# Kernel tuning notes

Hardware: AMD Instinct MI355X
Metric: run time of the kernel (lower is better)

The kernel has to match this reference:

```python
import jax, jax.numpy as jnp
import numpy as np

B, C, W, H = 4, 128, 64, 64
CK = 32  # f/g projection channels


def setup_inputs() -> dict:
    key = jax.random.key(0)
    ks = jax.random.split(key, 8)
    s_in = 1.0 / np.sqrt(C)
    return {
        "x": jax.random.normal(ks[0], (B, C, W, H), dtype=jnp.float32),
        "Wf": jax.random.normal(ks[1], (CK, C), dtype=jnp.float32) * s_in,
        "bf": jnp.zeros((CK,), dtype=jnp.float32),
        "Wg": jax.random.normal(ks[2], (CK, C), dtype=jnp.float32) * s_in,
        "bg": jnp.zeros((CK,), dtype=jnp.float32),
        "Wh": jax.random.normal(ks[3], (C, C), dtype=jnp.float32) * s_in,
        "bh": jnp.zeros((C,), dtype=jnp.float32),
        "gamma": jax.random.normal(ks[4], (1,), dtype=jnp.float32) * 0.1,
    }


def reference(x, Wf, bf, Wg, bg, Wh, bh, gamma):
    b, c, w, h = x.shape
    n = w * h
    xf = x.reshape(b, c, n)                                  # [B,C,N]
    # 1x1 convs == per-pixel linear projections
    f = jnp.einsum('oc,bcn->bon', Wf, xf) + bf[None, :, None]  # [B,32,N]
    g = jnp.einsum('oc,bcn->bon', Wg, xf) + bg[None, :, None]  # [B,32,N]
    v = jnp.einsum('oc,bcn->bon', Wh, xf) + bh[None, :, None]  # [B,C,N]
    # attention = softmax(f^T g) over last dim (g positions), as in the torch code
    att = jax.nn.softmax(jnp.einsum('bkn,bkm->bnm', f, g), axis=-1)  # [B,N,N]
    # self_attention = h @ attention  (contract over f-position axis)
    sa = jnp.einsum('bcn,bnm->bcm', v, att).reshape(b, c, w, h)
    return gamma[0] * sa + x
```

## Files before the change

kernel.cpp:

```cpp
#include <hip/hip_runtime.h>
#include <hip/hip_bf16.h>

#define BB 4
#define CC 128
#define NN 4096
#define CK 32
#define L2E 1.442695040888963f

typedef __attribute__((ext_vector_type(8))) short short8v;
typedef __attribute__((ext_vector_type(4))) float float4v;

__device__ inline ushort f2bf(float f) {
    union { __hip_bfloat16 h; ushort u; } cv;
    cv.h = __float2bfloat16(f);
    return cv.u;
}
__device__ inline float bf2f(ushort u) {
    union { uint u; float f; } cv;
    cv.u = ((uint)u) << 16;
    return cv.f;
}
__device__ inline uint pk2(float lo, float hi) {
    return ((uint)f2bf(lo)) | ((uint)f2bf(hi) << 16);
}
__device__ __forceinline__ void gll16(const void* g, void* l) {
    __builtin_amdgcn_global_load_lds(
        (const __attribute__((address_space(1))) void*)g,
        (__attribute__((address_space(3))) void*)l, 16, 0, 0);
}

__global__ __launch_bounds__(1024) void proj_kernel(
    const float* __restrict__ x,
    const float* __restrict__ Wf, const float* __restrict__ bf,
    const float* __restrict__ Wg, const float* __restrict__ bg,
    const float* __restrict__ Wh, const float* __restrict__ bh,
    const float* __restrict__ gamma,
    ushort* __restrict__ ft, ushort* __restrict__ gt, ushort* __restrict__ vh)
{
    __shared__ float xs[CC][64];
    const int t  = threadIdx.x;
    const int n0 = blockIdx.x * 64;
    const int b  = blockIdx.y;
    const float* xb = x + (size_t)b * CC * NN + n0;

    {
        const int j  = t & 63;
        const int cb = t >> 6;
        #pragma unroll
        for (int i = 0; i < 8; ++i)
            xs[cb + 16 * i][j] = xb[(size_t)(cb + 16 * i) * NN + j];
    }
    __syncthreads();

    const int jq = t & 15;
    const int og = (t >> 4) & 15;
    const int i3 = t >> 8;

    const float* wrow[3];
    float biasv[3];
    int   mode[3], oc[3];
    #pragma unroll
    for (int ii = 0; ii < 3; ++ii) {
        const int i = i3 * 3 + ii;
        if (i < 2)      { oc[ii] = og + 16 * i;       wrow[ii] = Wf + oc[ii] * CC; biasv[ii] = bf[oc[ii]]; mode[ii] = 0; }
        else if (i < 4) { oc[ii] = og + 16 * (i - 2); wrow[ii] = Wg + oc[ii] * CC; biasv[ii] = bg[oc[ii]]; mode[ii] = 1; }
        else            { oc[ii] = og + 16 * (i - 4); wrow[ii] = Wh + oc[ii] * CC; biasv[ii] = bh[oc[ii]]; mode[ii] = 2; }
    }

    float acc[3][4];
    #pragma unroll
    for (int ii = 0; ii < 3; ++ii)
        #pragma unroll
        for (int jj = 0; jj < 4; ++jj) acc[ii][jj] = 0.f;

    #pragma unroll 4
    for (int c4 = 0; c4 < 32; ++c4) {
        float4 wv[3];
        #pragma unroll
        for (int ii = 0; ii < 3; ++ii)
            wv[ii] = *reinterpret_cast<const float4*>(&wrow[ii][c4 * 4]);
        #pragma unroll
        for (int q = 0; q < 4; ++q) {
            const float4 xv = *reinterpret_cast<const float4*>(&xs[c4 * 4 + q][jq * 4]);
            #pragma unroll
            for (int ii = 0; ii < 3; ++ii) {
                const float wq = (q == 0) ? wv[ii].x : (q == 1) ? wv[ii].y
                               : (q == 2) ? wv[ii].z : wv[ii].w;
                acc[ii][0] += wq * xv.x;
                acc[ii][1] += wq * xv.y;
                acc[ii][2] += wq * xv.z;
                acc[ii][3] += wq * xv.w;
            }
        }
    }

    const float sgn = (gamma[0] < 0.f) ? -1.f : 1.f;
    const int n_base = n0 + jq * 4;
    #pragma unroll
    for (int ii = 0; ii < 3; ++ii) {
        if (mode[ii] == 0) {
            #pragma unroll
            for (int jj = 0; jj < 4; ++jj)
                ft[((size_t)b * NN + n_base + jj) * CK + oc[ii]] =
                    f2bf((acc[ii][jj] + biasv[ii]) * L2E);
        } else if (mode[ii] == 1) {
            #pragma unroll
            for (int jj = 0; jj < 4; ++jj)
                gt[((size_t)b * NN + n_base + jj) * CK + oc[ii]] = f2bf(acc[ii][jj] + biasv[ii]);
        } else {
            ushort4 pkv;
            pkv.x = f2bf(sgn * (acc[ii][0] + biasv[ii]));
            pkv.y = f2bf(sgn * (acc[ii][1] + biasv[ii]));
            pkv.z = f2bf(sgn * (acc[ii][2] + biasv[ii]));
            pkv.w = f2bf(sgn * (acc[ii][3] + biasv[ii]));
            *reinterpret_cast<ushort4*>(&vh[((size_t)b * CC + oc[ii]) * NN + n_base]) = pkv;
        }
    }
}

__global__ __launch_bounds__(256) void pass1_kernel(
    const ushort* __restrict__ ft, const ushort* __restrict__ gt,
    float* __restrict__ Dpart)
{
    const int t   = threadIdx.x;
    const int w   = t >> 6;
    const int l   = t & 63;
    const int g16 = l >> 4;
    const int l16 = l & 15;
    const int n0  = blockIdx.x * 64;
    const int b   = blockIdx.y;
    const int mz  = blockIdx.z;

    const ushort* ftb = ft + (size_t)b * NN * CK;
    const ushort* gtb = gt + (size_t)b * NN * CK;

    const short8v afrag = *reinterpret_cast<const short8v*>(
        &ftb[(size_t)(n0 + 16 * w + l16) * CK + 8 * g16]);

    const float4v zf = {0.f, 0.f, 0.f, 0.f};
    float d0 = 0.f, d1 = 0.f, d2 = 0.f, d3 = 0.f;
    const int m0 = mz * 512;

    short8v bfA = *reinterpret_cast<const short8v*>(
        &gtb[(size_t)(m0 + l16) * CK + 8 * g16]);
    #pragma unroll 1
    for (int mt = 0; mt < 32; mt += 2) {
        const short8v bfB = *reinterpret_cast<const short8v*>(
            &gtb[(size_t)(m0 + (mt + 1) * 16 + l16) * CK + 8 * g16]);
        float4v s = __builtin_amdgcn_mfma_f32_16x16x32_bf16(afrag, bfA, zf, 0, 0, 0);
        d0 += __builtin_amdgcn_exp2f(s[0]); d1 += __builtin_amdgcn_exp2f(s[1]);
        d2 += __builtin_amdgcn_exp2f(s[2]); d3 += __builtin_amdgcn_exp2f(s[3]);
        bfA = *reinterpret_cast<const short8v*>(
            &gtb[(size_t)(m0 + (((mt + 2) & 31)) * 16 + l16) * CK + 8 * g16]);
        float4v s2 = __builtin_amdgcn_mfma_f32_16x16x32_bf16(afrag, bfB, zf, 0, 0, 0);
        d0 += __builtin_amdgcn_exp2f(s2[0]); d1 += __builtin_amdgcn_exp2f(s2[1]);
        d2 += __builtin_amdgcn_exp2f(s2[2]); d3 += __builtin_amdgcn_exp2f(s2[3]);
    }
    #pragma unroll
    for (int msk = 1; msk <= 8; msk <<= 1) {
        d0 += __shfl_xor(d0, msk);
        d1 += __shfl_xor(d1, msk);
        d2 += __shfl_xor(d2, msk);
        d3 += __shfl_xor(d3, msk);
    }
    if (l16 < 4) {
        const int n = n0 + 16 * w + 4 * g16 + l16;
        const float v = (l16 == 0) ? d0 : (l16 == 1) ? d1 : (l16 == 2) ? d2 : d3;
        Dpart[((size_t)b * NN + n) * 8 + mz] = v;
    }
}

__global__ __launch_bounds__(256) void reduce_kernel(
    const float* __restrict__ Dpart, float* __restrict__ sc,
    const float* __restrict__ gamma)
{
    const int i = blockIdx.x * 256 + threadIdx.x;
    const float4 a4 = *reinterpret_cast<const float4*>(&Dpart[(size_t)i * 8]);
    const float4 b4 = *reinterpret_cast<const float4*>(&Dpart[(size_t)i * 8 + 4]);
    const float D = (a4.x + a4.y + a4.z + a4.w) + (b4.x + b4.y + b4.z + b4.w);
    sc[i] = fabsf(gamma[0]) / D;
}

__global__ __launch_bounds__(256) void vscale_kernel(
    ushort* __restrict__ vh, const float* __restrict__ sc)
{
    const size_t i8   = (size_t)blockIdx.x * 256 + threadIdx.x;
    const size_t base = i8 * 8;
    const int    n    = (int)(base & (NN - 1));
    const int    b    = (int)(base / ((size_t)CC * NN));

    ushort4 v0 = *reinterpret_cast<const ushort4*>(&vh[base]);
    ushort4 v1 = *reinterpret_cast<const ushort4*>(&vh[base + 4]);
    const float4 s0 = *reinterpret_cast<const float4*>(&sc[(size_t)b * NN + n]);
    const float4 s1 = *reinterpret_cast<const float4*>(&sc[(size_t)b * NN + n + 4]);

    v0.x = f2bf(bf2f(v0.x) * s0.x);
    v0.y = f2bf(bf2f(v0.y) * s0.y);
    v0.z = f2bf(bf2f(v0.z) * s0.z);
    v0.w = f2bf(bf2f(v0.w) * s0.w);
    v1.x = f2bf(bf2f(v1.x) * s1.x);
    v1.y = f2bf(bf2f(v1.y) * s1.y);
    v1.z = f2bf(bf2f(v1.z) * s1.z);
    v1.w = f2bf(bf2f(v1.w) * s1.w);

    *reinterpret_cast<ushort4*>(&vh[base])     = v0;
    *reinterpret_cast<ushort4*>(&vh[base + 4]) = v1;
}

#define WSTR  16384
#define VBUF  8192

__global__ __launch_bounds__(512) void pass2_kernel(
    const ushort* __restrict__ ft, const ushort* __restrict__ gt,
    const ushort* __restrict__ vh,
    const float* __restrict__ x, float* __restrict__ out)
{
    __shared__ __align__(16) char smem[8 * WSTR];

    const int t   = threadIdx.x;
    const int w   = t >> 6;
    const int l   = t & 63;
    const int g16 = l >> 4;
    const int l16 = l & 15;
    const int mq  = w & 1;
    const int nq  = w >> 1;

    const int bid = blockIdx.x;
    const int xcd = bid & 7;
    const int b   = xcd >> 1;
    const int m0  = ((bid >> 3) + 32 * (xcd & 1)) * 64;

    const ushort* ftb = ft + (size_t)b * NN * CK;
    const ushort* gtb = gt + (size_t)b * NN * CK;
    const ushort* vhb = vh + (size_t)b * CC * NN;

    char* wsm = smem + w * WSTR;

    short8v gfrag[2];
    #pragma unroll
    for (int tm = 0; tm < 2; ++tm)
        gfrag[tm] = *reinterpret_cast<const short8v*>(
            &gtb[(size_t)(m0 + 32 * mq + 16 * tm + l16) * CK + 8 * g16]);

    const float4v zf = {0.f, 0.f, 0.f, 0.f};
    float4v acc[8][2];
    #pragma unroll
    for (int tc = 0; tc < 8; ++tc)
        #pragma unroll
        for (int tm = 0; tm < 2; ++tm) acc[tc][tm] = zf;

    const int nbase = nq * 1024;
    const int rr = l >> 2, cp = l & 3;

#define STAGE(n0_, bo_) do {                                                   \
    _Pragma("unroll")                                                          \
    for (int j = 0; j < 8; ++j) {                                              \
        const int row = j * 16 + rr;                                           \
        gll16(vhb + (size_t)row * NN + (n0_)                                   \
                  + (((2 * cp) ^ (row & 6)) << 2),                             \
              wsm + (bo_) + j * 1024);                                         \
    }                                                                          \
} while (0)

    STAGE(nbase, 0);
    asm volatile("s_waitcnt vmcnt(0)" ::: "memory");

    int bo = 0;
    #pragma unroll 1
    for (int st = 0; st < 32; ++st) {
        const int n0 = nbase + st * 32;

        const short8v af0 = *reinterpret_cast<const short8v*>(
            &ftb[(size_t)(n0 + l16) * CK + 8 * g16]);
        const short8v af1 = *reinterpret_cast<const short8v*>(
            &ftb[(size_t)(n0 + 16 + l16) * CK + 8 * g16]);

        if (st < 31) {
            STAGE(n0 + 32, bo ^ VBUF);
            asm volatile("s_waitcnt vmcnt(8)" ::: "memory");
        } else {
            asm volatile("s_waitcnt vmcnt(0)" ::: "memory");
        }

        const char* Vb = wsm + bo;

        union { uint u[4]; short8v s; } pf[2];
        #pragma unroll
        for (int tm = 0; tm < 2; ++tm) {
            float4v s0 = __builtin_amdgcn_mfma_f32_16x16x32_bf16(af0, gfrag[tm], zf, 0, 0, 0);
            float4v s1 = __builtin_amdgcn_mfma_f32_16x16x32_bf16(af1, gfrag[tm], zf, 0, 0, 0);
            pf[tm].u[0] = pk2(__builtin_amdgcn_exp2f(s0[0]), __builtin_amdgcn_exp2f(s0[1]));
            pf[tm].u[1] = pk2(__builtin_amdgcn_exp2f(s0[2]), __builtin_amdgcn_exp2f(s0[3]));
            pf[tm].u[2] = pk2(__builtin_amdgcn_exp2f(s1[0]), __builtin_amdgcn_exp2f(s1[1]));
            pf[tm].u[3] = pk2(__builtin_amdgcn_exp2f(s1[2]), __builtin_amdgcn_exp2f(s1[3]));
        }

        #pragma unroll
        for (int tc = 0; tc < 8; ++tc) {
            const int cl = 16 * tc + l16;
            const uint2 va  = *reinterpret_cast<const uint2*>(
                Vb + cl * 64 + 8 * (g16 ^ (cl & 6)));
            const uint2 vb2 = *reinterpret_cast<const uint2*>(
                Vb + cl * 64 + 8 * ((4 + g16) ^ (cl & 6)));
            union { uint u[4]; short8v s; } av;
            av.u[0] = va.x;  av.u[1] = va.y;
            av.u[2] = vb2.x; av.u[3] = vb2.y;
            acc[tc][0] = __builtin_amdgcn_mfma_f32_16x16x32_bf16(av.s, pf[0].s, acc[tc][0], 0, 0, 0);
            acc[tc][1] = __builtin_amdgcn_mfma_f32_16x16x32_bf16(av.s, pf[1].s, acc[tc][1], 0, 0, 0);
        }
        bo ^= VBUF;
    }
#undef STAGE

    __syncthreads();
    float4v* rl = (float4v*)smem;
    if (nq != 0) {
        const int slot = (nq - 1) * 2 + mq;
        #pragma unroll
        for (int tc = 0; tc < 8; ++tc)
            #pragma unroll
            for (int tm = 0; tm < 2; ++tm)
                rl[(slot * 16 + tc * 2 + tm) * 64 + l] = acc[tc][tm];
    }
    __syncthreads();
    if (nq == 0) {
        const float* xb = x   + (size_t)b * CC * NN;
        float*       ob = out + (size_t)b * CC * NN;
        #pragma unroll
        for (int tc = 0; tc < 8; ++tc) {
            #pragma unroll
            for (int tm = 0; tm < 2; ++tm) {
                const int fi = tc * 2 + tm;
                float4v s = acc[tc][tm]
                          + rl[((mq) * 16 + fi) * 64 + l]
                          + rl[((2 + mq) * 16 + fi) * 64 + l]
                          + rl[((4 + mq) * 16 + fi) * 64 + l];
                const int cb = 16 * tc + 4 * g16;
                const int m  = m0 + 32 * mq + 16 * tm + l16;
                #pragma unroll
                for (int r = 0; r < 4; ++r) {
                    const size_t idx = (size_t)(cb + r) * NN + m;
                    ob[idx] = s[r] + xb[idx];
                }
            }
        }
    }
}

extern "C" void kernel_launch(void* const* d_in, const int* in_sizes, int n_in,
                              void* d_out, int out_size, void* d_ws, size_t ws_size,
                              hipStream_t stream)
{
    const float* x     = (const float*)d_in[0];
    const float* Wf    = (const float*)d_in[1];
    const float* bf    = (const float*)d_in[2];
    const float* Wg    = (const float*)d_in[3];
    const float* bg    = (const float*)d_in[4];
    const float* Wh    = (const float*)d_in[5];
    const float* bh    = (const float*)d_in[6];
    const float* gamma = (const float*)d_in[7];

    ushort* ft = (ushort*)d_ws;
    ushort* gt = ft + (size_t)BB * NN * CK;
    ushort* vh = gt + (size_t)BB * NN * CK;
    float* Dpart = (float*)(vh + (size_t)BB * CC * NN);
    float* sc    = Dpart + (size_t)BB * NN * 8;

    float* out = (float*)d_out;

    proj_kernel<<<dim3(NN / 64, BB), 1024, 0, stream>>>(x, Wf, bf, Wg, bg, Wh, bh, gamma, ft, gt, vh);
    pass1_kernel<<<dim3(NN / 64, BB, 8), 256, 0, stream>>>(ft, gt, Dpart);
    reduce_kernel<<<dim3(BB * NN / 256), 256, 0, stream>>>(Dpart, sc, gamma);
    vscale_kernel<<<dim3(BB * CC * NN / 8 / 256), 256, 0, stream>>>(vh, sc);
    pass2_kernel<<<dim3(256), 512, 0, stream>>>(ft, gt, vh, x, out);
}
```

Baseline: 83.53 us.

## Split pass2 work by channel halves, double grid, and unroll double-buffer loop

The pass2 kernel now gives each wave pair a 32-position m-tile split across two channel halves, where before each wave owned a slice of a 64-position tile. This halves the per-wave accumulators and LDS staging and doubles the grid to 512 blocks, with launch bounds requesting two blocks per CU for better occupancy on a 256-CU device. The main loop is unrolled by two with fixed double-buffer offsets, and the f-fragment loads are prefetched alongside the V staging. The trade-off is that exp/score MFMAs are recomputed by both channel-half waves, doubling that work.

```diff
diff --git a/kernel.cpp b/kernel.cpp
--- a/kernel.cpp
+++ b/kernel.cpp
@@ -207,10 +207,10 @@
     *reinterpret_cast<ushort4*>(&vh[base + 4]) = v1;
 }
 
-#define WSTR  16384
-#define VBUF  8192
-
-__global__ __launch_bounds__(512) void pass2_kernel(
+#define WSTR  8192
+#define VBUF  4096
+
+__global__ __launch_bounds__(512, 2) void pass2_kernel(
     const ushort* __restrict__ ft, const ushort* __restrict__ gt,
     const ushort* __restrict__ vh,
     const float* __restrict__ x, float* __restrict__ out)
@@ -222,13 +222,13 @@
     const int l   = t & 63;
     const int g16 = l >> 4;
     const int l16 = l & 15;
-    const int mq  = w & 1;
+    const int ch  = w & 1;
     const int nq  = w >> 1;
 
     const int bid = blockIdx.x;
     const int xcd = bid & 7;
     const int b   = xcd >> 1;
-    const int m0  = ((bid >> 3) + 32 * (xcd & 1)) * 64;
+    const int m0  = ((bid >> 3) + 64 * (xcd & 1)) * 32;
 
     const ushort* ftb = ft + (size_t)b * NN * CK;
     const ushort* gtb = gt + (size_t)b * NN * CK;
@@ -240,12 +240,12 @@
     #pragma unroll
     for (int tm = 0; tm < 2; ++tm)
         gfrag[tm] = *reinterpret_cast<const short8v*>(
-            &gtb[(size_t)(m0 + 32 * mq + 16 * tm + l16) * CK + 8 * g16]);
+            &gtb[(size_t)(m0 + 16 * tm + l16) * CK + 8 * g16]);
 
     const float4v zf = {0.f, 0.f, 0.f, 0.f};
-    float4v acc[8][2];
-    #pragma unroll
-    for (int tc = 0; tc < 8; ++tc)
+    float4v acc[4][2];
+    #pragma unroll
+    for (int tc = 0; tc < 4; ++tc)
         #pragma unroll
         for (int tm = 0; tm < 2; ++tm) acc[tc][tm] = zf;
 
@@ -254,89 +254,97 @@
 
 #define STAGE(n0_, bo_) do {                                                   \
     _Pragma("unroll")                                                          \
-    for (int j = 0; j < 8; ++j) {                                              \
+    for (int j = 0; j < 4; ++j) {                                              \
         const int row = j * 16 + rr;                                           \
-        gll16(vhb + (size_t)row * NN + (n0_)                                   \
+        gll16(vhb + (size_t)(64 * ch + row) * NN + (n0_)                       \
                   + (((2 * cp) ^ (row & 6)) << 2),                             \
               wsm + (bo_) + j * 1024);                                         \
     }                                                                          \
 } while (0)
 
+#define AFLOAD(A0, A1, n0_) do {                                               \
+    A0 = *reinterpret_cast<const short8v*>(                                    \
+        &ftb[(size_t)((n0_) + l16) * CK + 8 * g16]);                           \
+    A1 = *reinterpret_cast<const short8v*>(                                    \
+        &ftb[(size_t)((n0_) + 16 + l16) * CK + 8 * g16]);                      \
+} while (0)
+
+#define COMPUTE(bo_, A0, A1) do {                                              \
+    const char* Vb = wsm + (bo_);                                              \
+    union { uint u[4]; short8v s; } pf[2];                                     \
+    _Pragma("unroll")                                                          \
+    for (int tm = 0; tm < 2; ++tm) {                                           \
+        float4v s0 = __builtin_amdgcn_mfma_f32_16x16x32_bf16(A0, gfrag[tm], zf, 0, 0, 0); \
+        float4v s1 = __builtin_amdgcn_mfma_f32_16x16x32_bf16(A1, gfrag[tm], zf, 0, 0, 0); \
+        pf[tm].u[0] = pk2(__builtin_amdgcn_exp2f(s0[0]), __builtin_amdgcn_exp2f(s0[1])); \
+        pf[tm].u[1] = pk2(__builtin_amdgcn_exp2f(s0[2]), __builtin_amdgcn_exp2f(s0[3])); \
+        pf[tm].u[2] = pk2(__builtin_amdgcn_exp2f(s1[0]), __builtin_amdgcn_exp2f(s1[1])); \
+        pf[tm].u[3] = pk2(__builtin_amdgcn_exp2f(s1[2]), __builtin_amdgcn_exp2f(s1[3])); \
+    }                                                                          \
+    _Pragma("unroll")                                                          \
+    for (int tc = 0; tc < 4; ++tc) {                                           \
+        const int cl = 16 * tc + l16;                                          \
+        const uint2 va  = *reinterpret_cast<const uint2*>(                     \
+            Vb + cl * 64 + 8 * (g16 ^ (cl & 6)));                              \
+        const uint2 vb2 = *reinterpret_cast<const uint2*>(                     \
+            Vb + cl * 64 + 8 * ((4 + g16) ^ (cl & 6)));                        \
+        union { uint u[4]; short8v s; } av;                                    \
+        av.u[0] = va.x;  av.u[1] = va.y;                                       \
+        av.u[2] = vb2.x; av.u[3] = vb2.y;                                      \
+        acc[tc][0] = __builtin_amdgcn_mfma_f32_16x16x32_bf16(av.s, pf[0].s, acc[tc][0], 0, 0, 0); \
+        acc[tc][1] = __builtin_amdgcn_mfma_f32_16x16x32_bf16(av.s, pf[1].s, acc[tc][1], 0, 0, 0); \
+    }                                                                          \
+} while (0)
+
+    short8v afA0, afA1, afB0, afB1;
+
     STAGE(nbase, 0);
+    AFLOAD(afA0, afA1, nbase);
     asm volatile("s_waitcnt vmcnt(0)" ::: "memory");
 
-    int bo = 0;
     #pragma unroll 1
-    for (int st = 0; st < 32; ++st) {
-        const int n0 = nbase + st * 32;
-
-        const short8v af0 = *reinterpret_cast<const short8v*>(
-            &ftb[(size_t)(n0 + l16) * CK + 8 * g16]);
-        const short8v af1 = *reinterpret_cast<const short8v*>(
-            &ftb[(size_t)(n0 + 16 + l16) * CK + 8 * g16]);
-
-        if (st < 31) {
-            STAGE(n0 + 32, bo ^ VBUF);
-            asm volatile("s_waitcnt vmcnt(8)" ::: "memory");
-        } else {
-            asm volatile("s_waitcnt vmcnt(0)" ::: "memory");
-        }
-
-        const char* Vb = wsm + bo;
-
-        union { uint u[4]; short8v s; } pf[2];
-        #pragma unroll
-        for (int tm = 0; tm < 2; ++tm) {
-            float4v s0 = __builtin_amdgcn_mfma_f32_16x16x32_bf16(af0, gfrag[tm], zf, 0, 0, 0);
-            float4v s1 = __builtin_amdgcn_mfma_f32_16x16x32_bf16(af1, gfrag[tm], zf, 0, 0, 0);
-            pf[tm].u[0] = pk2(__builtin_amdgcn_exp2f(s0[0]), __builtin_amdgcn_exp2f(s0[1]));
-            pf[tm].u[1] = pk2(__builtin_amdgcn_exp2f(s0[2]), __builtin_amdgcn_exp2f(s0[3]));
-            pf[tm].u[2] = pk2(__builtin_amdgcn_exp2f(s1[0]), __builtin_amdgcn_exp2f(s1[1]));
-            pf[tm].u[3] = pk2(__builtin_amdgcn_exp2f(s1[2]), __builtin_amdgcn_exp2f(s1[3]));
-        }
-
-        #pragma unroll
-        for (int tc = 0; tc < 8; ++tc) {
-            const int cl = 16 * tc + l16;
-            const uint2 va  = *reinterpret_cast<const uint2*>(
-                Vb + cl * 64 + 8 * (g16 ^ (cl & 6)));
-            const uint2 vb2 = *reinterpret_cast<const uint2*>(
-                Vb + cl * 64 + 8 * ((4 + g16) ^ (cl & 6)));
-            union { uint u[4]; short8v s; } av;
-            av.u[0] = va.x;  av.u[1] = va.y;
-            av.u[2] = vb2.x; av.u[3] = vb2.y;
-            acc[tc][0] = __builtin_amdgcn_mfma_f32_16x16x32_bf16(av.s, pf[0].s, acc[tc][0], 0, 0, 0);
-            acc[tc][1] = __builtin_amdgcn_mfma_f32_16x16x32_bf16(av.s, pf[1].s, acc[tc][1], 0, 0, 0);
-        }
-        bo ^= VBUF;
+    for (int st = 0; st < 32; st += 2) {
+        const int n1 = nbase + ((st + 1) & 31) * 32;
+        STAGE(n1, VBUF);
+        AFLOAD(afB0, afB1, n1);
+        asm volatile("s_waitcnt vmcnt(6)" ::: "memory");
+        COMPUTE(0, afA0, afA1);
+
+        const int n2 = nbase + ((st + 2) & 31) * 32;
+        STAGE(n2, 0);
+        AFLOAD(afA0, afA1, n2);
+        asm volatile("s_waitcnt vmcnt(6)" ::: "memory");
+        COMPUTE(VBUF, afB0, afB1);
     }
 #undef STAGE
+#undef AFLOAD
+#undef COMPUTE
 
     __syncthreads();
     float4v* rl = (float4v*)smem;
     if (nq != 0) {
-        const int slot = (nq - 1) * 2 + mq;
-        #pragma unroll
-        for (int tc = 0; tc < 8; ++tc)
+        const int slot = (nq - 1) * 2 + ch;
+        #pragma unroll
+        for (int tc = 0; tc < 4; ++tc)
             #pragma unroll
             for (int tm = 0; tm < 2; ++tm)
-                rl[(slot * 16 + tc * 2 + tm) * 64 + l] = acc[tc][tm];
+                rl[(slot * 8 + tc * 2 + tm) * 64 + l] = acc[tc][tm];
     }
     __syncthreads();
     if (nq == 0) {
         const float* xb = x   + (size_t)b * CC * NN;
         float*       ob = out + (size_t)b * CC * NN;
         #pragma unroll
-        for (int tc = 0; tc < 8; ++tc) {
+        for (int tc = 0; tc < 4; ++tc) {
             #pragma unroll
             for (int tm = 0; tm < 2; ++tm) {
                 const int fi = tc * 2 + tm;
                 float4v s = acc[tc][tm]
-                          + rl[((mq) * 16 + fi) * 64 + l]
-                          + rl[((2 + mq) * 16 + fi) * 64 + l]
-                          + rl[((4 + mq) * 16 + fi) * 64 + l];
-                const int cb = 16 * tc + 4 * g16;
-                const int m  = m0 + 32 * mq + 16 * tm + l16;
+                          + rl[((ch) * 8 + fi) * 64 + l]
+                          + rl[((2 + ch) * 8 + fi) * 64 + l]
+                          + rl[((4 + ch) * 8 + fi) * 64 + l];
+                const int cb = 64 * ch + 16 * tc + 4 * g16;
+                const int m  = m0 + 16 * tm + l16;
                 #pragma unroll
                 for (int r = 0; r < 4; ++r) {
                     const size_t idx = (size_t)(cb + r) * NN + m;
@@ -372,5 +380,5 @@
     pass1_kernel<<<dim3(NN / 64, BB, 8), 256, 0, stream>>>(ft, gt, Dpart);
     reduce_kernel<<<dim3(BB * NN / 256), 256, 0, stream>>>(Dpart, sc, gamma);
     vscale_kernel<<<dim3(BB * CC * NN / 8 / 256), 256, 0, stream>>>(vh, sc);
-    pass2_kernel<<<dim3(256), 512, 0, stream>>>(ft, gt, vh, x, out);
-}
+    pass2_kernel<<<dim3(512), 512, 0, stream>>>(ft, gt, vh, x, out);
+}
```

After: 92.18 us. 10.4% more time.

## Split pass2 work across 16 waves by channel halves with tree reduction

Applied to the files above, without the earlier changes.

Raises pass2 blocks from 8 to 16 waves. Each wave now owns one half of the channels for all 64 query columns and handles 512 key positions instead of 1024. The cross-wave reduction of partial accumulators becomes a three-level tree through shared memory. The aim is more latency hiding per CU and less V staging per wave. In exchange, each wave recomputes the exp scores for all four m-tiles, and the reduction adds several more block barriers.

```diff
diff --git a/kernel.cpp b/kernel.cpp
--- a/kernel.cpp
+++ b/kernel.cpp
@@ -207,22 +207,22 @@
     *reinterpret_cast<ushort4*>(&vh[base + 4]) = v1;
 }
 
-#define WSTR  16384
-#define VBUF  8192
-
-__global__ __launch_bounds__(512) void pass2_kernel(
+#define WSTR  8192
+#define VBUF  4096
+
+__global__ __launch_bounds__(1024) void pass2_kernel(
     const ushort* __restrict__ ft, const ushort* __restrict__ gt,
     const ushort* __restrict__ vh,
     const float* __restrict__ x, float* __restrict__ out)
 {
-    __shared__ __align__(16) char smem[8 * WSTR];
+    __shared__ __align__(16) char smem[16 * WSTR];
 
     const int t   = threadIdx.x;
     const int w   = t >> 6;
     const int l   = t & 63;
     const int g16 = l >> 4;
     const int l16 = l & 15;
-    const int mq  = w & 1;
+    const int ch  = w & 1;
     const int nq  = w >> 1;
 
     const int bid = blockIdx.x;
@@ -236,27 +236,27 @@
 
     char* wsm = smem + w * WSTR;
 
-    short8v gfrag[2];
-    #pragma unroll
-    for (int tm = 0; tm < 2; ++tm)
+    short8v gfrag[4];
+    #pragma unroll
+    for (int tm = 0; tm < 4; ++tm)
         gfrag[tm] = *reinterpret_cast<const short8v*>(
-            &gtb[(size_t)(m0 + 32 * mq + 16 * tm + l16) * CK + 8 * g16]);
+            &gtb[(size_t)(m0 + 16 * tm + l16) * CK + 8 * g16]);
 
     const float4v zf = {0.f, 0.f, 0.f, 0.f};
-    float4v acc[8][2];
-    #pragma unroll
-    for (int tc = 0; tc < 8; ++tc)
-        #pragma unroll
-        for (int tm = 0; tm < 2; ++tm) acc[tc][tm] = zf;
-
-    const int nbase = nq * 1024;
+    float4v acc[4][4];
+    #pragma unroll
+    for (int tc = 0; tc < 4; ++tc)
+        #pragma unroll
+        for (int tm = 0; tm < 4; ++tm) acc[tc][tm] = zf;
+
+    const int nbase = nq * 512;
     const int rr = l >> 2, cp = l & 3;
 
 #define STAGE(n0_, bo_) do {                                                   \
     _Pragma("unroll")                                                          \
-    for (int j = 0; j < 8; ++j) {                                              \
+    for (int j = 0; j < 4; ++j) {                                              \
         const int row = j * 16 + rr;                                           \
-        gll16(vhb + (size_t)row * NN + (n0_)                                   \
+        gll16(vhb + (size_t)(64 * ch + row) * NN + (n0_)                       \
                   + (((2 * cp) ^ (row & 6)) << 2),                             \
               wsm + (bo_) + j * 1024);                                         \
     }                                                                          \
@@ -267,7 +267,7 @@
 
     int bo = 0;
     #pragma unroll 1
-    for (int st = 0; st < 32; ++st) {
+    for (int st = 0; st < 16; ++st) {
         const int n0 = nbase + st * 32;
 
         const short8v af0 = *reinterpret_cast<const short8v*>(
@@ -275,18 +275,18 @@
         const short8v af1 = *reinterpret_cast<const short8v*>(
             &ftb[(size_t)(n0 + 16 + l16) * CK + 8 * g16]);
 
-        if (st < 31) {
+        if (st < 15) {
             STAGE(n0 + 32, bo ^ VBUF);
-            asm volatile("s_waitcnt vmcnt(8)" ::: "memory");
+            asm volatile("s_waitcnt vmcnt(4)" ::: "memory");
         } else {
             asm volatile("s_waitcnt vmcnt(0)" ::: "memory");
         }
 
         const char* Vb = wsm + bo;
 
-        union { uint u[4]; short8v s; } pf[2];
-        #pragma unroll
-        for (int tm = 0; tm < 2; ++tm) {
+        union { uint u[4]; short8v s; } pf[4];
+        #pragma unroll
+        for (int tm = 0; tm < 4; ++tm) {
             float4v s0 = __builtin_amdgcn_mfma_f32_16x16x32_bf16(af0, gfrag[tm], zf, 0, 0, 0);
             float4v s1 = __builtin_amdgcn_mfma_f32_16x16x32_bf16(af1, gfrag[tm], zf, 0, 0, 0);
             pf[tm].u[0] = pk2(__builtin_amdgcn_exp2f(s0[0]), __builtin_amdgcn_exp2f(s0[1]));
@@ -296,7 +296,7 @@
         }
 
         #pragma unroll
-        for (int tc = 0; tc < 8; ++tc) {
+        for (int tc = 0; tc < 4; ++tc) {
             const int cl = 16 * tc + l16;
             const uint2 va  = *reinterpret_cast<const uint2*>(
                 Vb + cl * 64 + 8 * (g16 ^ (cl & 6)));
@@ -305,38 +305,70 @@
             union { uint u[4]; short8v s; } av;
             av.u[0] = va.x;  av.u[1] = va.y;
             av.u[2] = vb2.x; av.u[3] = vb2.y;
-            acc[tc][0] = __builtin_amdgcn_mfma_f32_16x16x32_bf16(av.s, pf[0].s, acc[tc][0], 0, 0, 0);
-            acc[tc][1] = __builtin_amdgcn_mfma_f32_16x16x32_bf16(av.s, pf[1].s, acc[tc][1], 0, 0, 0);
+            #pragma unroll
+            for (int tm = 0; tm < 4; ++tm)
+                acc[tc][tm] = __builtin_amdgcn_mfma_f32_16x16x32_bf16(av.s, pf[tm].s, acc[tc][tm], 0, 0, 0);
         }
         bo ^= VBUF;
     }
 #undef STAGE
 
-    __syncthreads();
     float4v* rl = (float4v*)smem;
-    if (nq != 0) {
-        const int slot = (nq - 1) * 2 + mq;
-        #pragma unroll
-        for (int tc = 0; tc < 8; ++tc)
-            #pragma unroll
-            for (int tm = 0; tm < 2; ++tm)
-                rl[(slot * 16 + tc * 2 + tm) * 64 + l] = acc[tc][tm];
+    __syncthreads();
+    if (nq >= 4) {
+        const int slot = (nq - 4) * 2 + ch;
+        #pragma unroll
+        for (int tc = 0; tc < 4; ++tc)
+            #pragma unroll
+            for (int tm = 0; tm < 4; ++tm)
+                rl[(slot * 16 + tc * 4 + tm) * 64 + l] = acc[tc][tm];
+    }
+    __syncthreads();
+    if (nq < 4) {
+        const int slot = nq * 2 + ch;
+        #pragma unroll
+        for (int tc = 0; tc < 4; ++tc)
+            #pragma unroll
+            for (int tm = 0; tm < 4; ++tm)
+                acc[tc][tm] += rl[(slot * 16 + tc * 4 + tm) * 64 + l];
+    }
+    __syncthreads();
+    if (nq == 2 || nq == 3) {
+        const int slot = (nq - 2) * 2 + ch;
+        #pragma unroll
+        for (int tc = 0; tc < 4; ++tc)
+            #pragma unroll
+            for (int tm = 0; tm < 4; ++tm)
+                rl[(slot * 16 + tc * 4 + tm) * 64 + l] = acc[tc][tm];
+    }
+    __syncthreads();
+    if (nq < 2) {
+        const int slot = nq * 2 + ch;
+        #pragma unroll
+        for (int tc = 0; tc < 4; ++tc)
+            #pragma unroll
+            for (int tm = 0; tm < 4; ++tm)
+                acc[tc][tm] += rl[(slot * 16 + tc * 4 + tm) * 64 + l];
+    }
+    __syncthreads();
+    if (nq == 1) {
+        #pragma unroll
+        for (int tc = 0; tc < 4; ++tc)
+            #pragma unroll
+            for (int tm = 0; tm < 4; ++tm)
+                rl[(ch * 16 + tc * 4 + tm) * 64 + l] = acc[tc][tm];
     }
     __syncthreads();
     if (nq == 0) {
         const float* xb = x   + (size_t)b * CC * NN;
         float*       ob = out + (size_t)b * CC * NN;
         #pragma unroll
-        for (int tc = 0; tc < 8; ++tc) {
-            #pragma unroll
-            for (int tm = 0; tm < 2; ++tm) {
-                const int fi = tc * 2 + tm;
-                float4v s = acc[tc][tm]
-                          + rl[((mq) * 16 + fi) * 64 + l]
-                          + rl[((2 + mq) * 16 + fi) * 64 + l]
-                          + rl[((4 + mq) * 16 + fi) * 64 + l];
-                const int cb = 16 * tc + 4 * g16;
-                const int m  = m0 + 32 * mq + 16 * tm + l16;
+        for (int tc = 0; tc < 4; ++tc) {
+            #pragma unroll
+            for (int tm = 0; tm < 4; ++tm) {
+                float4v s = acc[tc][tm] + rl[(ch * 16 + tc * 4 + tm) * 64 + l];
+                const int cb = 64 * ch + 16 * tc + 4 * g16;
+                const int m  = m0 + 16 * tm + l16;
                 #pragma unroll
                 for (int r = 0; r < 4; ++r) {
                     const size_t idx = (size_t)(cb + r) * NN + m;
@@ -372,5 +404,5 @@
     pass1_kernel<<<dim3(NN / 64, BB, 8), 256, 0, stream>>>(ft, gt, Dpart);
     reduce_kernel<<<dim3(BB * NN / 256), 256, 0, stream>>>(Dpart, sc, gamma);
     vscale_kernel<<<dim3(BB * CC * NN / 8 / 256), 256, 0, stream>>>(vh, sc);
-    pass2_kernel<<<dim3(256), 512, 0, stream>>>(ft, gt, vh, x, out);
-}
+    pass2_kernel<<<dim3(256), 1024, 0, stream>>>(ft, gt, vh, x, out);
+}
```

Result: no change. 84.29 us (+0.9%).
